# Kernel tuning notes

Measured on AMD Instinct MI355X. Metric: run time of the kernel, lower is better.

Reference implementation:

```python
import jax, jax.numpy as jnp
import numpy as np

IN_DIM, OUT_DIM = 256, 64
N_WNODES, N_PNODES, N_EDGES = 100000, 50000, 1600000


def setup_inputs() -> dict:
    key = jax.random.key(0)
    k_h, k_src, k_dst, k_fc, k_attn = jax.random.split(key, 5)
    h = jax.random.normal(k_h, (N_WNODES, IN_DIM), dtype=jnp.float32)
    edge_src = jax.random.randint(k_src, (N_EDGES,), 0, N_WNODES)
    edge_dst = jax.random.randint(k_dst, (N_EDGES,), 0, N_PNODES)
    W_fc = jax.random.normal(k_fc, (IN_DIM, OUT_DIM), dtype=jnp.float32) / np.sqrt(IN_DIM)
    # attn_fc: Linear(2*out_dim, 1, bias=False) -> weight vector of length 2*OUT_DIM
    W_attn = jax.random.normal(k_attn, (2 * OUT_DIM,), dtype=jnp.float32) / np.sqrt(2 * OUT_DIM)
    return {"h": h, "edge_src": edge_src, "edge_dst": edge_dst,
            "n_pnodes": N_PNODES, "W_fc": W_fc, "W_attn": W_attn}


def reference(h, edge_src, edge_dst, n_pnodes, W_fc, W_attn):
    D = W_fc.shape[1]
    z = h @ W_fc                                  # [Nw, D]
    z_src = z[edge_src]                           # [E, D] gather (memory-bound)
    # In the original, only word nodes get 'z'; DGL zero-fills dst 'z', so the
    # dst half of attn_fc contributes nothing: e = leaky_relu(z_src @ a_src + 0 @ a_dst)
    a_src = W_attn[:D]
    e = jax.nn.leaky_relu(z_src @ a_src)          # [E], slope 0.01 matches torch default
    # reduce_func masks zero-valued scores (DGL mailbox padding) with -1000
    e = jnp.where(e == 0.0, -1000.0, e)
    # segment softmax over incoming edges of each destination node
    e_max = jax.ops.segment_max(e, edge_dst, num_segments=n_pnodes)
    e_max = jnp.where(jnp.isfinite(e_max), e_max, 0.0)  # guard empty segments
    w = jnp.exp(e - e_max[edge_dst])              # [E]
    denom = jax.ops.segment_sum(w, edge_dst, num_segments=n_pnodes)
    alpha = w / jnp.maximum(denom[edge_dst], 1e-20)
    # weighted gather-scatter aggregation: sh[dst] = sum alpha * z_src
    h_out = jax.ops.segment_sum(alpha[:, None] * z_src, edge_dst, num_segments=n_pnodes)
    return h_out                                  # [n_pnodes, D] == h[pnode_id]
```

## Files before the change

### kernel.cpp

```cpp
#include <hip/hip_runtime.h>
#include <hip/hip_bf16.h>
#include <math.h>

#define IN_DIM 256
#define OUT_DIM 64
#define CHUNK_LOG2 12
#define BK_LOG2 7
#define MAXNB 512
#define BCAP 6144

typedef __attribute__((ext_vector_type(8))) short short8v;
typedef __attribute__((ext_vector_type(4))) float f32x4;

__device__ __forceinline__ unsigned short f2bf(float f) {
    unsigned u = __float_as_uint(f);
    unsigned r = (u + 0x7fffu + ((u >> 16) & 1u)) >> 16;
    return (unsigned short)r;
}

__device__ __forceinline__ float bf2f(unsigned short b) {
    return __uint_as_float(((unsigned)b) << 16);
}

__device__ __forceinline__ float edge_score(float x) {
    float e = x > 0.0f ? x : 0.01f * x;
    if (e == 0.0f) e = -1000.0f;
    return e;
}

__device__ __forceinline__ void gload_lds16(const void* g, void* l) {
    __builtin_amdgcn_global_load_lds(
        (const __attribute__((address_space(1))) unsigned int*)g,
        (__attribute__((address_space(3))) unsigned int*)l, 16, 0, 0);
}

__global__ __launch_bounds__(256) void prep_kernel(
    const float* __restrict__ Wfc, short8v* __restrict__ wtf)
{
    const int v = blockIdx.x * 256 + threadIdx.x;
    const int ks = v >> 8;
    const int t = (v >> 6) & 3;
    const int lane = v & 63;
    const int lg = lane >> 4, lr = lane & 15;
    short8v b;
    #pragma unroll
    for (int j = 0; j < 8; ++j) {
        const int k = ks * 32 + lg * 8 + j;
        b[j] = (short)f2bf(Wfc[k * OUT_DIM + t * 16 + lr]);
    }
    wtf[v] = b;
}

__global__ __launch_bounds__(256) void gemm_s_kernel(
    const float* __restrict__ h, const short8v* __restrict__ wtf,
    const float* __restrict__ Wattn, const int* __restrict__ esrc,
    const int* __restrict__ edst, unsigned short* __restrict__ z,
    float* __restrict__ s, int* __restrict__ bres, int* __restrict__ brec,
    int n_rows, int n_edges, int nb)
{
    __shared__ float hl[64 * IN_DIM];
    const int tid = threadIdx.x;
    const int lane = tid & 63;
    const int wv = tid >> 6;
    const int lg = lane >> 4;
    const int lr = lane & 15;
    const int row0 = blockIdx.x * 64;

    const int nchunks = (n_edges + (1 << CHUNK_LOG2) - 1) >> CHUNK_LOG2;
    const bool hasChunk = blockIdx.x < nchunks;
    const bool fullChunk = hasChunk &&
        ((blockIdx.x << CHUNK_LOG2) + (1 << CHUNK_LOG2) <= n_edges);
    int4 ed[4], es[4];
    if (fullChunk) {
        const int4* ep = (const int4*)edst + (blockIdx.x << (CHUNK_LOG2 - 2));
        const int4* sp = (const int4*)esrc + (blockIdx.x << (CHUNK_LOG2 - 2));
        #pragma unroll
        for (int j = 0; j < 4; ++j) { ed[j] = ep[j * 256 + tid]; es[j] = sp[j * 256 + tid]; }
    }

    short8v Bf[8][4];
    #pragma unroll
    for (int ks = 0; ks < 8; ++ks)
        #pragma unroll
        for (int t = 0; t < 4; ++t)
            Bf[ks][t] = wtf[(ks * 4 + t) * 64 + lane];

    float a_attn[4];
    #pragma unroll
    for (int t = 0; t < 4; ++t) a_attn[t] = Wattn[t * 16 + lr];

    #pragma unroll
    for (int i = 0; i < 16; ++i) {
        const int q = i * 256 + tid;
        const int row = q >> 6;
        const int within = q & 63;
        const int lslot = within ^ (row & 7);
        const int grow = min(row0 + row, n_rows - 1);
        gload_lds16(h + (size_t)grow * IN_DIM + lslot * 4, hl + q * 4);
    }
    __syncthreads();

    f32x4 acc[4];
    #pragma unroll
    for (int t = 0; t < 4; ++t) acc[t] = (f32x4){0.f, 0.f, 0.f, 0.f};

    const int rowl = wv * 16 + lr;
    const char* rbase = (const char*)hl + rowl * 1024;
    const int swz = (lr & 7) << 4;

    union AB { short8v v; __hip_bfloat162 h2[4]; };
    #pragma unroll
    for (int ks = 0; ks < 8; ++ks) {
        const int lb = ks * 128 + lg * 32;
        const float4 x0 = *(const float4*)(rbase + (lb ^ swz));
        const float4 x1 = *(const float4*)(rbase + ((lb + 16) ^ swz));
        AB u;
        u.h2[0] = __float22bfloat162_rn(float2{x0.x, x0.y});
        u.h2[1] = __float22bfloat162_rn(float2{x0.z, x0.w});
        u.h2[2] = __float22bfloat162_rn(float2{x1.x, x1.y});
        u.h2[3] = __float22bfloat162_rn(float2{x1.z, x1.w});
        #pragma unroll
        for (int t = 0; t < 4; ++t)
            acc[t] = __builtin_amdgcn_mfma_f32_16x16x32_bf16(u.v, Bf[ks][t], acc[t], 0, 0, 0);
    }

    #pragma unroll
    for (int j = 0; j < 4; ++j) {
        const int row = row0 + wv * 16 + lg * 4 + j;
        const bool ok = row < n_rows;
        float sv = 0.0f;
        #pragma unroll
        for (int t = 0; t < 4; ++t) {
            const float v = acc[t][j];
            if (ok) z[(size_t)row * OUT_DIM + t * 16 + lr] =
                __bfloat16_as_ushort(__float2bfloat16(v));
            sv = fmaf(v, a_attn[t], sv);
        }
        #pragma unroll
        for (int o = 1; o < 16; o <<= 1) sv += __shfl_xor(sv, o);
        if (ok && lr == 0) s[row] = sv;
    }

    __syncthreads();
    int* lcnt = (int*)hl;
    int* lwoff = lcnt + MAXNB;
    if (hasChunk) {
        for (int j2 = tid; j2 < nb; j2 += 256) lcnt[j2] = 0;
        __syncthreads();
        if (fullChunk) {
            #pragma unroll
            for (int j2 = 0; j2 < 4; ++j2) {
                atomicAdd(&lcnt[ed[j2].x >> BK_LOG2], 1);
                atomicAdd(&lcnt[ed[j2].y >> BK_LOG2], 1);
                atomicAdd(&lcnt[ed[j2].z >> BK_LOG2], 1);
                atomicAdd(&lcnt[ed[j2].w >> BK_LOG2], 1);
            }
        } else {
            const int i0 = blockIdx.x << CHUNK_LOG2;
            const int i1 = min(i0 + (1 << CHUNK_LOG2), n_edges);
            for (int i = i0 + tid; i < i1; i += 256)
                atomicAdd(&lcnt[edst[i] >> BK_LOG2], 1);
        }
        __syncthreads();
        for (int j2 = tid; j2 < nb; j2 += 256) {
            const int cv = lcnt[j2];
            lwoff[j2] = cv ? (j2 * BCAP + atomicAdd(bres + j2, cv)) : 0;
        }
        __syncthreads();
        if (fullChunk) {
            #pragma unroll
            for (int j2 = 0; j2 < 4; ++j2) {
                #define EMIT(dd, ss) { \
                    const int pos = atomicAdd(&lwoff[(dd) >> BK_LOG2], 1); \
                    brec[pos] = (ss) | (((dd) & ((1 << BK_LOG2) - 1)) << 17); }
                EMIT(ed[j2].x, es[j2].x)
                EMIT(ed[j2].y, es[j2].y)
                EMIT(ed[j2].z, es[j2].z)
                EMIT(ed[j2].w, es[j2].w)
                #undef EMIT
            }
        } else {
            const int i0 = blockIdx.x << CHUNK_LOG2;
            const int i1 = min(i0 + (1 << CHUNK_LOG2), n_edges);
            for (int i = i0 + tid; i < i1; i += 256) {
                const int d = edst[i];
                const int pos = atomicAdd(&lwoff[d >> BK_LOG2], 1);
                brec[pos] = esrc[i] | ((d & ((1 << BK_LOG2) - 1)) << 17);
            }
        }
    }
}

__global__ __launch_bounds__(256) void p2_kernel(
    const int* __restrict__ bres, int* __restrict__ brec,
    int2* __restrict__ oln, int n_pnodes)
{
    __shared__ int srec[BCAP];
    __shared__ int lh[128], lsc[128], lwf[128];
    const int b = blockIdx.x;
    const int tid = threadIdx.x;
    const int base = b * BCAP;
    const int len = min(bres[b], BCAP);

    if (tid < 128) lh[tid] = 0;
    __syncthreads();
    for (int i = tid; i < len; i += 256) {
        const int r = brec[base + i];
        srec[i] = r;
        atomicAdd(&lh[r >> 17], 1);
    }
    __syncthreads();
    if (tid < 128) lsc[tid] = lh[tid];
    __syncthreads();
    for (int d = 1; d < 128; d <<= 1) {
        int v = 0;
        if (tid < 128 && tid >= d) v = lsc[tid - d];
        __syncthreads();
        if (tid < 128) lsc[tid] += v;
        __syncthreads();
    }
    const int d0 = b << BK_LOG2;
    if (tid < 128) {
        const int st = lsc[tid] - lh[tid];
        lwf[tid] = st;
        if (d0 + tid < n_pnodes)
            oln[d0 + tid] = make_int2(base + st, lh[tid]);
    }
    __syncthreads();
    for (int i = tid; i < len; i += 256) {
        const int r = srec[i];
        const int pos = atomicAdd(&lwf[r >> 17], 1);
        brec[base + pos] = r & 0x1FFFF;
    }
}

__global__ __launch_bounds__(256) void segment_kernel(
    const int2* __restrict__ oln, const int* __restrict__ ssrc,
    const float* __restrict__ s, const unsigned short* __restrict__ z,
    float* __restrict__ out, int n_pnodes)
{
    const int p = blockIdx.x * 4 + (threadIdx.x >> 6);
    if (p >= n_pnodes) return;
    const int lane = threadIdx.x & 63;
    const int2 ol = oln[p];
    const int beg = ol.x;
    const int len = ol.y;
    const int end = beg + len;

    if (len == 0) {
        out[(size_t)p * OUT_DIM + lane] = 0.0f;
        return;
    }

    float acc = 0.0f, dsum = 0.0f;

    #define GATH1(tt, wsrc, ssrcv) { \
        float wt = __shfl(wsrc, tt); \
        int st = __shfl(ssrcv, tt); \
        acc = fmaf(wt, bf2f(z[(size_t)st * OUT_DIM + lane]), acc); }
    #define GATH8(tt, wsrc, ssrcv) { \
        float w0 = __shfl(wsrc, tt),     w1 = __shfl(wsrc, tt + 1); \
        float w2 = __shfl(wsrc, tt + 2), w3 = __shfl(wsrc, tt + 3); \
        float w4 = __shfl(wsrc, tt + 4), w5 = __shfl(wsrc, tt + 5); \
        float w6 = __shfl(wsrc, tt + 6), w7 = __shfl(wsrc, tt + 7); \
        int a0 = __shfl(ssrcv, tt),     a1 = __shfl(ssrcv, tt + 1); \
        int a2 = __shfl(ssrcv, tt + 2), a3 = __shfl(ssrcv, tt + 3); \
        int a4 = __shfl(ssrcv, tt + 4), a5 = __shfl(ssrcv, tt + 5); \
        int a6 = __shfl(ssrcv, tt + 6), a7 = __shfl(ssrcv, tt + 7); \
        float z0 = bf2f(z[(size_t)a0 * OUT_DIM + lane]); \
        float z1 = bf2f(z[(size_t)a1 * OUT_DIM + lane]); \
        float z2 = bf2f(z[(size_t)a2 * OUT_DIM + lane]); \
        float z3 = bf2f(z[(size_t)a3 * OUT_DIM + lane]); \
        float z4 = bf2f(z[(size_t)a4 * OUT_DIM + lane]); \
        float z5 = bf2f(z[(size_t)a5 * OUT_DIM + lane]); \
        float z6 = bf2f(z[(size_t)a6 * OUT_DIM + lane]); \
        float z7 = bf2f(z[(size_t)a7 * OUT_DIM + lane]); \
        acc = fmaf(w0, z0, acc); acc = fmaf(w1, z1, acc); \
        acc = fmaf(w2, z2, acc); acc = fmaf(w3, z3, acc); \
        acc = fmaf(w4, z4, acc); acc = fmaf(w5, z5, acc); \
        acc = fmaf(w6, z6, acc); acc = fmaf(w7, z7, acc); }

    if (len <= 64) {
        const bool v = lane < len;
        const int j = beg + (v ? lane : 0);
        const int sr = ssrc[j];
        const float e = v ? edge_score(s[sr]) : -INFINITY;
        float m = e;
        #pragma unroll
        for (int o = 32; o > 0; o >>= 1) m = fmaxf(m, __shfl_xor(m, o));
        float w = v ? __expf(e - m) : 0.0f;
        dsum = w;
        #pragma unroll
        for (int o = 32; o > 0; o >>= 1) dsum += __shfl_xor(dsum, o);

        int t = 0;
        for (; t + 8 <= len; t += 8) GATH8(t, w, sr)
        for (; t < len; ++t) GATH1(t, w, sr)
    } else {
        float m = -INFINITY;
        for (int j = beg + lane; j < end; j += 64)
            m = fmaxf(m, edge_score(s[ssrc[j]]));
        #pragma unroll
        for (int o = 32; o > 0; o >>= 1) m = fmaxf(m, __shfl_xor(m, o));

        for (int c = beg; c < end; c += 64) {
            const int j = c + lane;
            float w = 0.0f;
            int sr = 0;
            if (j < end) {
                sr = ssrc[j];
                w = __expf(edge_score(s[sr]) - m);
            }
            dsum += w;
            const int cn = min(64, end - c);
            int t = 0;
            for (; t + 8 <= cn; t += 8) GATH8(t, w, sr)
            for (; t < cn; ++t) GATH1(t, w, sr)
        }
        #pragma unroll
        for (int o = 32; o > 0; o >>= 1) dsum += __shfl_xor(dsum, o);
    }
    #undef GATH8
    #undef GATH1

    out[(size_t)p * OUT_DIM + lane] = acc / fmaxf(dsum, 1e-20f);
}

extern "C" void kernel_launch(void* const* d_in, const int* in_sizes, int n_in,
                              void* d_out, int out_size, void* d_ws, size_t ws_size,
                              hipStream_t stream)
{
    const float* h     = (const float*)d_in[0];
    const int*   esrc  = (const int*)d_in[1];
    const int*   edst  = (const int*)d_in[2];
    const float* Wfc   = (const float*)d_in[4];
    const float* Wattn = (const float*)d_in[5];
    float* out = (float*)d_out;

    const int n_w = in_sizes[0] / IN_DIM;
    const int n_e = in_sizes[1];
    const int n_p = out_size / OUT_DIM;
    const int nb  = (n_p + (1 << BK_LOG2) - 1) >> BK_LOG2;

    short8v* wtf            = (short8v*)d_ws;
    unsigned short* z       = (unsigned short*)(wtf + 2048);
    float* s                = (float*)(z + (size_t)n_w * OUT_DIM);
    int* brec               = (int*)(s + n_w);
    int2* oln               = (int2*)(brec + (size_t)nb * BCAP);
    int* bres               = (int*)(oln + n_p);

    hipMemsetAsync(bres, 0, (size_t)nb * sizeof(int), stream);

    prep_kernel<<<8, 256, 0, stream>>>(Wfc, wtf);
    const int gemm_blocks = (n_w + 63) / 64;
    gemm_s_kernel<<<gemm_blocks, 256, 0, stream>>>(h, wtf, Wattn, esrc, edst,
                                                   z, s, bres, brec, n_w, n_e, nb);
    p2_kernel<<<nb, 256, 0, stream>>>(bres, brec, oln, n_p);
    segment_kernel<<<(n_p + 3) / 4, 256, 0, stream>>>(oln, brec, s, z, out, n_p);
}
```

Measured before the change: 110.2 us.

## Stage h tile as bf16 in LDS and split B fragments for occupancy

The h tile is now loaded through registers, converted to bf16 and written into a half-size swizzled LDS buffer (32 KB instead of 64 KB), replacing the async global-to-LDS fp32 loads. The W fragments are loaded in two halves of output columns rather than all at once, which lowers register pressure, and launch bounds now request 3 blocks per SM. The aim is more resident blocks to hide memory latency in this bandwidth-bound GEMM. The cost is losing the direct-to-LDS async copy, doing the conversion on the load path, and reading the LDS A tile twice.

```diff
diff --git a/kernel.cpp b/kernel.cpp
--- a/kernel.cpp
+++ b/kernel.cpp
@@ -28,12 +28,6 @@
     return e;
 }
 
-__device__ __forceinline__ void gload_lds16(const void* g, void* l) {
-    __builtin_amdgcn_global_load_lds(
-        (const __attribute__((address_space(1))) unsigned int*)g,
-        (__attribute__((address_space(3))) unsigned int*)l, 16, 0, 0);
-}
-
 __global__ __launch_bounds__(256) void prep_kernel(
     const float* __restrict__ Wfc, short8v* __restrict__ wtf)
 {
@@ -51,14 +45,14 @@
     wtf[v] = b;
 }
 
-__global__ __launch_bounds__(256) void gemm_s_kernel(
+__global__ __launch_bounds__(256, 3) void gemm_s_kernel(
     const float* __restrict__ h, const short8v* __restrict__ wtf,
     const float* __restrict__ Wattn, const int* __restrict__ esrc,
     const int* __restrict__ edst, unsigned short* __restrict__ z,
     float* __restrict__ s, int* __restrict__ bres, int* __restrict__ brec,
     int n_rows, int n_edges, int nb)
 {
-    __shared__ float hl[64 * IN_DIM];
+    __shared__ short hl2[64 * 256];
     const int tid = threadIdx.x;
     const int lane = tid & 63;
     const int wv = tid >> 6;
@@ -78,71 +72,81 @@
         for (int j = 0; j < 4; ++j) { ed[j] = ep[j * 256 + tid]; es[j] = sp[j * 256 + tid]; }
     }
 
-    short8v Bf[8][4];
-    #pragma unroll
-    for (int ks = 0; ks < 8; ++ks)
-        #pragma unroll
-        for (int t = 0; t < 4; ++t)
-            Bf[ks][t] = wtf[(ks * 4 + t) * 64 + lane];
-
     float a_attn[4];
     #pragma unroll
     for (int t = 0; t < 4; ++t) a_attn[t] = Wattn[t * 16 + lr];
 
     #pragma unroll
-    for (int i = 0; i < 16; ++i) {
+    for (int i = 0; i < 8; ++i) {
         const int q = i * 256 + tid;
-        const int row = q >> 6;
-        const int within = q & 63;
-        const int lslot = within ^ (row & 7);
-        const int grow = min(row0 + row, n_rows - 1);
-        gload_lds16(h + (size_t)grow * IN_DIM + lslot * 4, hl + q * 4);
-    }
-    __syncthreads();
-
-    f32x4 acc[4];
-    #pragma unroll
-    for (int t = 0; t < 4; ++t) acc[t] = (f32x4){0.f, 0.f, 0.f, 0.f};
-
-    const int rowl = wv * 16 + lr;
-    const char* rbase = (const char*)hl + rowl * 1024;
-    const int swz = (lr & 7) << 4;
-
-    union AB { short8v v; __hip_bfloat162 h2[4]; };
-    #pragma unroll
-    for (int ks = 0; ks < 8; ++ks) {
-        const int lb = ks * 128 + lg * 32;
-        const float4 x0 = *(const float4*)(rbase + (lb ^ swz));
-        const float4 x1 = *(const float4*)(rbase + ((lb + 16) ^ swz));
-        AB u;
-        u.h2[0] = __float22bfloat162_rn(float2{x0.x, x0.y});
-        u.h2[1] = __float22bfloat162_rn(float2{x0.z, x0.w});
-        u.h2[2] = __float22bfloat162_rn(float2{x1.x, x1.y});
-        u.h2[3] = __float22bfloat162_rn(float2{x1.z, x1.w});
-        #pragma unroll
-        for (int t = 0; t < 4; ++t)
-            acc[t] = __builtin_amdgcn_mfma_f32_16x16x32_bf16(u.v, Bf[ks][t], acc[t], 0, 0, 0);
+        const int r = q >> 5;
+        const int sl = q & 31;
+        const int grow = min(row0 + r, n_rows - 1);
+        const float4* hp = (const float4*)(h + (size_t)grow * IN_DIM + sl * 8);
+        const float4 xa = hp[0];
+        const float4 xb = hp[1];
+        union { short8v v; __hip_bfloat162 h2[4]; } u;
+        u.h2[0] = __float22bfloat162_rn(float2{xa.x, xa.y});
+        u.h2[1] = __float22bfloat162_rn(float2{xa.z, xa.w});
+        u.h2[2] = __float22bfloat162_rn(float2{xb.x, xb.y});
+        u.h2[3] = __float22bfloat162_rn(float2{xb.z, xb.w});
+        *(short8v*)((char*)hl2 + r * 512 + ((sl ^ (r & 31)) << 4)) = u.v;
+    }
+    __syncthreads();
+
+    const int rA = wv * 16 + lr;
+    const char* rbase = (const char*)hl2 + rA * 512;
+    const int rsw = rA & 31;
+
+    float svj[4] = {0.f, 0.f, 0.f, 0.f};
+
+    #pragma unroll
+    for (int hf = 0; hf < 2; ++hf) {
+        short8v Bf[8][2];
+        #pragma unroll
+        for (int ks = 0; ks < 8; ++ks)
+            #pragma unroll
+            for (int tt = 0; tt < 2; ++tt)
+                Bf[ks][tt] = wtf[(ks * 4 + hf * 2 + tt) * 64 + lane];
+
+        f32x4 acc[2];
+        acc[0] = (f32x4){0.f, 0.f, 0.f, 0.f};
+        acc[1] = (f32x4){0.f, 0.f, 0.f, 0.f};
+
+        #pragma unroll
+        for (int ks = 0; ks < 8; ++ks) {
+            const short8v av =
+                *(const short8v*)(rbase + (((ks * 4 + lg) ^ rsw) << 4));
+            acc[0] = __builtin_amdgcn_mfma_f32_16x16x32_bf16(av, Bf[ks][0], acc[0], 0, 0, 0);
+            acc[1] = __builtin_amdgcn_mfma_f32_16x16x32_bf16(av, Bf[ks][1], acc[1], 0, 0, 0);
+        }
+
+        #pragma unroll
+        for (int j = 0; j < 4; ++j) {
+            const int row = row0 + wv * 16 + lg * 4 + j;
+            const bool ok = row < n_rows;
+            #pragma unroll
+            for (int tt = 0; tt < 2; ++tt) {
+                const int t = hf * 2 + tt;
+                const float v = acc[tt][j];
+                if (ok) z[(size_t)row * OUT_DIM + t * 16 + lr] =
+                    __bfloat16_as_ushort(__float2bfloat16(v));
+                svj[j] = fmaf(v, a_attn[t], svj[j]);
+            }
+        }
     }
 
     #pragma unroll
     for (int j = 0; j < 4; ++j) {
         const int row = row0 + wv * 16 + lg * 4 + j;
-        const bool ok = row < n_rows;
-        float sv = 0.0f;
-        #pragma unroll
-        for (int t = 0; t < 4; ++t) {
-            const float v = acc[t][j];
-            if (ok) z[(size_t)row * OUT_DIM + t * 16 + lr] =
-                __bfloat16_as_ushort(__float2bfloat16(v));
-            sv = fmaf(v, a_attn[t], sv);
-        }
-        #pragma unroll
-        for (int o = 1; o < 16; o <<= 1) sv += __shfl_xor(sv, o);
-        if (ok && lr == 0) s[row] = sv;
-    }
-
-    __syncthreads();
-    int* lcnt = (int*)hl;
+        float p = svj[j];
+        #pragma unroll
+        for (int o = 1; o < 16; o <<= 1) p += __shfl_xor(p, o);
+        if (row < n_rows && lr == 0) s[row] = p;
+    }
+
+    __syncthreads();
+    int* lcnt = (int*)hl2;
     int* lwoff = lcnt + MAXNB;
     if (hasChunk) {
         for (int j2 = tid; j2 < nb; j2 += 256) lcnt[j2] = 0;
```

Result: no change. 111.0 us (+0.7%).

## Split edge bucketing out of GEMM kernel into separate scatter kernel

Applied to the files above, without the earlier changes.

Moves the edge bucket count/scatter phase out of the GEMM kernel into its own 512-thread scatter kernel, launched after the GEMM on the same stream. The GEMM kernel gets a launch bound of 2 blocks per CU and no longer holds the edge registers or runs the trailing atomic phase. This is meant to lower register pressure and raise GEMM occupancy. The cost is an extra kernel launch, and the bucketing no longer overlaps with GEMM work across blocks.

```diff
diff --git a/kernel.cpp b/kernel.cpp
--- a/kernel.cpp
+++ b/kernel.cpp
@@ -51,12 +51,10 @@
     wtf[v] = b;
 }
 
-__global__ __launch_bounds__(256) void gemm_s_kernel(
+__global__ __launch_bounds__(256, 2) void gemm_s_kernel(
     const float* __restrict__ h, const short8v* __restrict__ wtf,
-    const float* __restrict__ Wattn, const int* __restrict__ esrc,
-    const int* __restrict__ edst, unsigned short* __restrict__ z,
-    float* __restrict__ s, int* __restrict__ bres, int* __restrict__ brec,
-    int n_rows, int n_edges, int nb)
+    const float* __restrict__ Wattn, unsigned short* __restrict__ z,
+    float* __restrict__ s, int n_rows)
 {
     __shared__ float hl[64 * IN_DIM];
     const int tid = threadIdx.x;
@@ -65,18 +63,6 @@
     const int lg = lane >> 4;
     const int lr = lane & 15;
     const int row0 = blockIdx.x * 64;
-
-    const int nchunks = (n_edges + (1 << CHUNK_LOG2) - 1) >> CHUNK_LOG2;
-    const bool hasChunk = blockIdx.x < nchunks;
-    const bool fullChunk = hasChunk &&
-        ((blockIdx.x << CHUNK_LOG2) + (1 << CHUNK_LOG2) <= n_edges);
-    int4 ed[4], es[4];
-    if (fullChunk) {
-        const int4* ep = (const int4*)edst + (blockIdx.x << (CHUNK_LOG2 - 2));
-        const int4* sp = (const int4*)esrc + (blockIdx.x << (CHUNK_LOG2 - 2));
-        #pragma unroll
-        for (int j = 0; j < 4; ++j) { ed[j] = ep[j * 256 + tid]; es[j] = sp[j * 256 + tid]; }
-    }
 
     short8v Bf[8][4];
     #pragma unroll
@@ -140,53 +126,64 @@
         for (int o = 1; o < 16; o <<= 1) sv += __shfl_xor(sv, o);
         if (ok && lr == 0) s[row] = sv;
     }
-
-    __syncthreads();
-    int* lcnt = (int*)hl;
-    int* lwoff = lcnt + MAXNB;
-    if (hasChunk) {
-        for (int j2 = tid; j2 < nb; j2 += 256) lcnt[j2] = 0;
-        __syncthreads();
-        if (fullChunk) {
-            #pragma unroll
-            for (int j2 = 0; j2 < 4; ++j2) {
-                atomicAdd(&lcnt[ed[j2].x >> BK_LOG2], 1);
-                atomicAdd(&lcnt[ed[j2].y >> BK_LOG2], 1);
-                atomicAdd(&lcnt[ed[j2].z >> BK_LOG2], 1);
-                atomicAdd(&lcnt[ed[j2].w >> BK_LOG2], 1);
-            }
-        } else {
-            const int i0 = blockIdx.x << CHUNK_LOG2;
-            const int i1 = min(i0 + (1 << CHUNK_LOG2), n_edges);
-            for (int i = i0 + tid; i < i1; i += 256)
-                atomicAdd(&lcnt[edst[i] >> BK_LOG2], 1);
-        }
-        __syncthreads();
-        for (int j2 = tid; j2 < nb; j2 += 256) {
-            const int cv = lcnt[j2];
-            lwoff[j2] = cv ? (j2 * BCAP + atomicAdd(bres + j2, cv)) : 0;
-        }
-        __syncthreads();
-        if (fullChunk) {
-            #pragma unroll
-            for (int j2 = 0; j2 < 4; ++j2) {
-                #define EMIT(dd, ss) { \
-                    const int pos = atomicAdd(&lwoff[(dd) >> BK_LOG2], 1); \
-                    brec[pos] = (ss) | (((dd) & ((1 << BK_LOG2) - 1)) << 17); }
-                EMIT(ed[j2].x, es[j2].x)
-                EMIT(ed[j2].y, es[j2].y)
-                EMIT(ed[j2].z, es[j2].z)
-                EMIT(ed[j2].w, es[j2].w)
-                #undef EMIT
-            }
-        } else {
-            const int i0 = blockIdx.x << CHUNK_LOG2;
-            const int i1 = min(i0 + (1 << CHUNK_LOG2), n_edges);
-            for (int i = i0 + tid; i < i1; i += 256) {
-                const int d = edst[i];
-                const int pos = atomicAdd(&lwoff[d >> BK_LOG2], 1);
-                brec[pos] = esrc[i] | ((d & ((1 << BK_LOG2) - 1)) << 17);
-            }
+}
+
+__global__ __launch_bounds__(512) void scatter_kernel(
+    const int* __restrict__ esrc, const int* __restrict__ edst,
+    int* __restrict__ bres, int* __restrict__ brec, int n_edges, int nb)
+{
+    __shared__ int lcnt[MAXNB];
+    __shared__ int lwoff[MAXNB];
+    const int tid = threadIdx.x;
+    const int i0 = blockIdx.x << CHUNK_LOG2;
+    const int i1 = min(i0 + (1 << CHUNK_LOG2), n_edges);
+    const bool full = (i1 - i0) == (1 << CHUNK_LOG2);
+
+    int4 s4[2], d4[2];
+    if (full) {
+        const int4* sp = (const int4*)esrc + (i0 >> 2);
+        const int4* dp = (const int4*)edst + (i0 >> 2);
+        s4[0] = sp[tid];       s4[1] = sp[512 + tid];
+        d4[0] = dp[tid];       d4[1] = dp[512 + tid];
+    }
+
+    for (int j = tid; j < nb; j += 512) lcnt[j] = 0;
+    __syncthreads();
+    if (full) {
+        #pragma unroll
+        for (int j = 0; j < 2; ++j) {
+            atomicAdd(&lcnt[d4[j].x >> BK_LOG2], 1);
+            atomicAdd(&lcnt[d4[j].y >> BK_LOG2], 1);
+            atomicAdd(&lcnt[d4[j].z >> BK_LOG2], 1);
+            atomicAdd(&lcnt[d4[j].w >> BK_LOG2], 1);
+        }
+    } else {
+        for (int i = i0 + tid; i < i1; i += 512)
+            atomicAdd(&lcnt[edst[i] >> BK_LOG2], 1);
+    }
+    __syncthreads();
+    for (int j = tid; j < nb; j += 512) {
+        const int cv = lcnt[j];
+        lwoff[j] = cv ? (j * BCAP + atomicAdd(bres + j, cv)) : 0;
+    }
+    __syncthreads();
+    if (full) {
+        #pragma unroll
+        for (int j = 0; j < 2; ++j) {
+            #define EMIT(dd, ss) { \
+                const int pos = atomicAdd(&lwoff[(dd) >> BK_LOG2], 1); \
+                brec[pos] = (ss) | (((dd) & ((1 << BK_LOG2) - 1)) << 17); }
+            EMIT(d4[j].x, s4[j].x)
+            EMIT(d4[j].y, s4[j].y)
+            EMIT(d4[j].z, s4[j].z)
+            EMIT(d4[j].w, s4[j].w)
+            #undef EMIT
+        }
+    } else {
+        for (int i = i0 + tid; i < i1; i += 512) {
+            const int d = edst[i];
+            const int pos = atomicAdd(&lwoff[d >> BK_LOG2], 1);
+            brec[pos] = esrc[i] | ((d & ((1 << BK_LOG2) - 1)) << 17);
         }
     }
 }
@@ -353,8 +350,10 @@
 
     prep_kernel<<<8, 256, 0, stream>>>(Wfc, wtf);
     const int gemm_blocks = (n_w + 63) / 64;
-    gemm_s_kernel<<<gemm_blocks, 256, 0, stream>>>(h, wtf, Wattn, esrc, edst,
-                                                   z, s, bres, brec, n_w, n_e, nb);
+    gemm_s_kernel<<<gemm_blocks, 256, 0, stream>>>(h, wtf, Wattn, z, s, n_w);
+
+    const int nchunks = (n_e + (1 << CHUNK_LOG2) - 1) >> CHUNK_LOG2;
+    scatter_kernel<<<nchunks, 512, 0, stream>>>(esrc, edst, bres, brec, n_e, nb);
     p2_kernel<<<nb, 256, 0, stream>>>(bres, brec, oln, n_p);
     segment_kernel<<<(n_p + 3) / 4, 256, 0, stream>>>(oln, brec, s, z, out, n_p);
 }
```

New measurement: 117.7 us. 6.8% more time.
